# Optimization experiments

Measured on AMD Instinct MI355X. Metric: run time of the kernel, lower is better.

Reference implementation:

```python
import jax, jax.numpy as jnp
import numpy as np

N_NODES = 100000
N_EDGES = 800000
HID = 128
LN_EPS = 1e-5


def _mlp2(x, w1, b1, w2, b2):
    # Linear -> ReLU -> Linear
    return jax.nn.relu(x @ w1 + b1) @ w2 + b2


def setup_inputs() -> dict:
    key = jax.random.key(0)
    ks = jax.random.split(key, 12)
    s = 1.0 / np.sqrt(3 * HID)
    s2 = 1.0 / np.sqrt(HID)
    return {
        "h": jax.random.normal(ks[0], (N_NODES, HID), dtype=jnp.float32),
        "edge_index": jax.random.randint(ks[1], (2, N_EDGES), 0, N_NODES, dtype=jnp.int64),
        "edge_x": jax.random.normal(ks[2], (N_EDGES, HID), dtype=jnp.float32),
        # edge_proj MLP (weights stored [in, out])
        "ep_w1": jax.random.uniform(ks[3], (3 * HID, HID), jnp.float32, -s, s),
        "ep_b1": jax.random.uniform(ks[4], (HID,), jnp.float32, -s, s),
        "ep_w2": jax.random.uniform(ks[5], (HID, HID), jnp.float32, -s2, s2),
        "ep_b2": jax.random.uniform(ks[6], (HID,), jnp.float32, -s2, s2),
        # update MLP
        "up_w1": jax.random.uniform(ks[7], (3 * HID, HID), jnp.float32, -s, s),
        "up_b1": jax.random.uniform(ks[8], (HID,), jnp.float32, -s, s),
        "up_w2": jax.random.uniform(ks[9], (HID, HID), jnp.float32, -s2, s2),
        "up_b2": jax.random.uniform(ks[10], (HID,), jnp.float32, -s2, s2),
        # LayerNorm affine
        "ln_g": jnp.ones((HID,), jnp.float32),
        "ln_b": jnp.zeros((HID,), jnp.float32),
    }


def reference(h, edge_index, edge_x, ep_w1, ep_b1, ep_w2, ep_b2,
              up_w1, up_b1, up_w2, up_b2, ln_g, ln_b):
    n = h.shape[0]
    src, dst = edge_index[0], edge_index[1]
    # edge gather + concat -> [E, 3H] -> message MLP -> [E, H]
    messages = _mlp2(jnp.concatenate([h[src], h[dst], edge_x], axis=-1),
                     ep_w1, ep_b1, ep_w2, ep_b2)
    # scatter-add aggregation for both directions
    incoming = jax.ops.segment_sum(messages, dst, num_segments=n)
    outgoing = jax.ops.segment_sum(messages, src, num_segments=n)
    # degree normalization (clamp min 1)
    ones = jnp.ones((edge_index.shape[1],), h.dtype)
    in_deg = jnp.maximum(jax.ops.segment_sum(ones, dst, num_segments=n), 1.0)[:, None]
    out_deg = jnp.maximum(jax.ops.segment_sum(ones, src, num_segments=n), 1.0)[:, None]
    updated = _mlp2(jnp.concatenate([h, incoming / in_deg, outgoing / out_deg], axis=-1),
                    up_w1, up_b1, up_w2, up_b2)
    # residual + LayerNorm
    x = h + updated
    mu = jnp.mean(x, axis=-1, keepdims=True)
    var = jnp.mean(jnp.square(x - mu), axis=-1, keepdims=True)
    return (x - mu) * jax.lax.rsqrt(var + LN_EPS) * ln_g + ln_b
```

## Files before the change

kernel.cpp:

```cpp
#include <hip/hip_runtime.h>
#include <stdint.h>

#define HIDD 128
#define NNODES 100000
#define NEDGES 800000
#define NSEG 196

typedef short s16x8 __attribute__((ext_vector_type(8)));
typedef float f32x4 __attribute__((ext_vector_type(4)));

__device__ __forceinline__ short f2bf(float f) {
  union { float f; unsigned u; } v; v.f = f;
  return (short)((v.u + 0x7fffu + ((v.u >> 16) & 1u)) >> 16);
}
__device__ __forceinline__ short4 cvt4(float4 v) {
  short4 s; s.x = f2bf(v.x); s.y = f2bf(v.y); s.z = f2bf(v.z); s.w = f2bf(v.w);
  return s;
}
__device__ __forceinline__ float bflo(unsigned w) {
  union { unsigned u; float f; } v; v.u = w << 16; return v.f;
}
__device__ __forceinline__ float bfhi(unsigned w) {
  union { unsigned u; float f; } v; v.u = w & 0xffff0000u; return v.f;
}
__device__ __forceinline__ unsigned pack2(float a, float b) {
  return ((unsigned)(unsigned short)f2bf(b) << 16) | (unsigned)(unsigned short)f2bf(a);
}
__device__ __forceinline__ f32x4 mfma16(s16x8 a, s16x8 b, f32x4 c) {
  return __builtin_amdgcn_mfma_f32_16x16x32_bf16(a, b, c, 0, 0, 0);
}
__device__ __forceinline__ void atomic_pk_bf16(unsigned short* addr, unsigned pk) {
  asm volatile("global_atomic_pk_add_bf16 %0, %1, off" :: "v"(addr), "v"(pk) : "memory");
}

__global__ void k_prep_h(const float4* __restrict__ h4, short4* __restrict__ hb4, int n4) {
  int stride = gridDim.x * blockDim.x;
  for (int i = blockIdx.x * blockDim.x + threadIdx.x; i < n4; i += stride)
    hb4[i] = cvt4(h4[i]);
}

__global__ void k_prep_w(const float* __restrict__ w1e, const float* __restrict__ w2e,
                         const float* __restrict__ w1u, const float* __restrict__ w2u,
                         short* __restrict__ w1et, short* __restrict__ w2et,
                         short* __restrict__ w1ut, short* __restrict__ w2ut) {
  int i = blockIdx.x * 256 + threadIdx.x;
  if (i < 49152) {
    int n = i / 384, k = i - n * 384;
    w1et[i] = f2bf(w1e[k * 128 + n]);
    w1ut[i] = f2bf(w1u[k * 128 + n]);
  } else {
    int j = i - 49152;
    if (j < 16384) {
      int n = j >> 7, k = j & 127;
      int oc = (n & ~31) + 2 * (n & 15) + ((n >> 4) & 1);
      w2et[j] = f2bf(w2e[k * 128 + oc]);
      w2ut[j] = f2bf(w2u[k * 128 + n]);
    }
  }
}

__global__ void k_hist(const int* __restrict__ eidx, int* __restrict__ cnt_s,
                       int* __restrict__ cnt_d) {
  int i = blockIdx.x * 256 + threadIdx.x;
  if (i < NEDGES) {
    atomicAdd(&cnt_s[eidx[i]], 1);
    atomicAdd(&cnt_d[eidx[NEDGES + i]], 1);
  }
}

__global__ void k_bsum(const int* __restrict__ cnt_d, const int* __restrict__ cnt_s,
                       int* __restrict__ bsum) {
  __shared__ int red[256];
  int gb = blockIdx.x, sel = gb >= NSEG, b = gb - sel * NSEG;
  const int* cnt = sel ? cnt_s : cnt_d;
  int t = threadIdx.x;
  int i0 = b * 512 + 2 * t;
  int a = (i0 < NNODES) ? cnt[i0] : 0;
  int c = (i0 + 1 < NNODES) ? cnt[i0 + 1] : 0;
  red[t] = a + c;
  __syncthreads();
  for (int d = 128; d > 0; d >>= 1) {
    if (t < d) red[t] += red[t + d];
    __syncthreads();
  }
  if (t == 0) bsum[gb] = red[0];
}

__global__ void k_soff(int* __restrict__ bsum, int* __restrict__ off_d,
                       int* __restrict__ off_s) {
  if (threadIdx.x == 0) {
    int tot = 0;
    for (int i = 0; i < NSEG; ++i) { int v = bsum[i]; bsum[i] = tot; tot += v; }
    off_d[NNODES] = tot;
  } else if (threadIdx.x == 1) {
    int tot = 0;
    for (int i = NSEG; i < 2 * NSEG; ++i) { int v = bsum[i]; bsum[i] = tot; tot += v; }
    off_s[NNODES] = tot;
  }
}

__global__ void k_sfin(const int* __restrict__ cnt_d, const int* __restrict__ cnt_s,
                       const int* __restrict__ bsum,
                       int* __restrict__ off_d, int* __restrict__ off_s,
                       int* __restrict__ cur_d, int* __restrict__ cur_s) {
  __shared__ int p[256];
  int gb = blockIdx.x, sel = gb >= NSEG, b = gb - sel * NSEG;
  const int* cnt = sel ? cnt_s : cnt_d;
  int* off = sel ? off_s : off_d;
  int* cur = sel ? cur_s : cur_d;
  int t = threadIdx.x;
  int i0 = b * 512 + 2 * t;
  int a = (i0 < NNODES) ? cnt[i0] : 0;
  int c = (i0 + 1 < NNODES) ? cnt[i0 + 1] : 0;
  p[t] = a + c;
  __syncthreads();
  for (int d = 1; d < 256; d <<= 1) {
    int v = (t >= d) ? p[t - d] : 0;
    __syncthreads();
    p[t] += v;
    __syncthreads();
  }
  int excl = (t ? p[t - 1] : 0) + bsum[gb];
  if (i0 < NNODES)     { off[i0] = excl;     cur[i0] = excl; }
  if (i0 + 1 < NNODES) { off[i0 + 1] = excl + a; cur[i0 + 1] = excl + a; }
}

__global__ void k_scat(const int* __restrict__ eidx, int* __restrict__ cur_s,
                       int* __restrict__ cur_d, int* __restrict__ slist,
                       int* __restrict__ dlist) {
  int i = blockIdx.x * 256 + threadIdx.x;
  if (i < NEDGES) {
    slist[atomicAdd(&cur_s[eidx[i]], 1)] = i;
    dlist[atomicAdd(&cur_d[eidx[NEDGES + i]], 1)] = i;
  }
}

__global__ __launch_bounds__(256, 2)
void k_edge2(const short* __restrict__ hb, const int* __restrict__ eidx,
             const float* __restrict__ ex,
             const short* __restrict__ w1t, const short* __restrict__ w2t,
             const float* __restrict__ b1g, const float* __restrict__ b2g,
             unsigned* __restrict__ msgd) {
  __shared__ __align__(16) short Xs[64][392];
  __shared__ __align__(16) short Hs[64][136];

  const int tid = threadIdx.x;
  const int wave = tid >> 6, lane = tid & 63;
  const int lg = lane >> 4, lr = lane & 15;
  const int koff = lg * 8;
  const int c0 = wave * 32 + lr, c1 = c0 + 16;
  const int pc0 = wave * 32 + 2 * lr;

  s16x8 wb1a[12], wb1b[12], wb2a[4], wb2b[4];
#pragma unroll
  for (int kk = 0; kk < 12; ++kk) {
    wb1a[kk] = *(const s16x8*)(w1t + c0 * 384 + kk * 32 + koff);
    wb1b[kk] = *(const s16x8*)(w1t + c1 * 384 + kk * 32 + koff);
  }
#pragma unroll
  for (int kk = 0; kk < 4; ++kk) {
    wb2a[kk] = *(const s16x8*)(w2t + c0 * 128 + kk * 32 + koff);
    wb2b[kk] = *(const s16x8*)(w2t + c1 * 128 + kk * 32 + koff);
  }
  const float bias1_0 = b1g[c0], bias1_1 = b1g[c1];
  const float bias2_0 = b2g[pc0], bias2_1 = b2g[pc0 + 1];

  for (int t = blockIdx.x; t < NEDGES / 64; t += gridDim.x) {
    const int base = t * 64;

    for (int u = tid; u < 64 * 32; u += 256) {
      int r = u >> 5, c = u & 31;
      int node = (c < 16) ? eidx[base + r] : eidx[NEDGES + base + r];
      *(int4*)&Xs[r][c * 8] = *(const int4*)(hb + (long)node * 128 + (c & 15) * 8);
    }
    for (int u = tid; u < 64 * 32; u += 256) {
      int r = u >> 5, q = u & 31;
      float4 v = *(const float4*)(ex + (long)(base + r) * 128 + q * 4);
      *(short4*)&Xs[r][256 + q * 4] = cvt4(v);
    }
    __syncthreads();

    f32x4 acc[4][2] = {};
#pragma unroll
    for (int kk = 0; kk < 12; ++kk) {
      int k0 = kk * 32 + koff;
#pragma unroll
      for (int m = 0; m < 4; ++m) {
        s16x8 a = *(const s16x8*)&Xs[m * 16 + lr][k0];
        acc[m][0] = mfma16(a, wb1a[kk], acc[m][0]);
        acc[m][1] = mfma16(a, wb1b[kk], acc[m][1]);
      }
    }
#pragma unroll
    for (int m = 0; m < 4; ++m)
#pragma unroll
      for (int r2 = 0; r2 < 4; ++r2) {
        int row = m * 16 + lg * 4 + r2;
        Hs[row][c0] = f2bf(fmaxf(acc[m][0][r2] + bias1_0, 0.f));
        Hs[row][c1] = f2bf(fmaxf(acc[m][1][r2] + bias1_1, 0.f));
      }
    __syncthreads();

    f32x4 acc2[4][2] = {};
#pragma unroll
    for (int kk = 0; kk < 4; ++kk) {
#pragma unroll
      for (int m = 0; m < 4; ++m) {
        s16x8 a = *(const s16x8*)&Hs[m * 16 + lr][kk * 32 + koff];
        acc2[m][0] = mfma16(a, wb2a[kk], acc2[m][0]);
        acc2[m][1] = mfma16(a, wb2b[kk], acc2[m][1]);
      }
    }
#pragma unroll
    for (int m = 0; m < 4; ++m)
#pragma unroll
      for (int r2 = 0; r2 < 4; ++r2) {
        int row = m * 16 + lg * 4 + r2;
        msgd[(long)(base + row) * 64 + wave * 16 + lr] =
            pack2(acc2[m][0][r2] + bias2_0, acc2[m][1][r2] + bias2_1);
      }
  }
}

__global__ __launch_bounds__(256, 2)
void k_node2(const float* __restrict__ h, const short* __restrict__ hb,
             const unsigned short* __restrict__ msg,
             const int* __restrict__ off_d, const int* __restrict__ dlist,
             const int* __restrict__ off_s, const int* __restrict__ slist,
             const short* __restrict__ w1t, const short* __restrict__ w2t,
             const float* __restrict__ b1g, const float* __restrict__ b2g,
             const float* __restrict__ lng, const float* __restrict__ lnb,
             float* __restrict__ out) {
  __shared__ __align__(16) char smem[67584];
  short (*Xs)[392] = (short (*)[392])smem;
  float (*Xf)[132] = (float (*)[132])smem;
  short (*Hs)[136] = (short (*)[136])(smem + 50176);

  const int tid = threadIdx.x;
  const int wave = tid >> 6, lane = tid & 63;
  const int lg = lane >> 4, lr = lane & 15;
  const int koff = lg * 8;
  const int c0 = wave * 32 + lr, c1 = c0 + 16;

  s16x8 wb1a[12], wb1b[12], wb2a[4], wb2b[4];
#pragma unroll
  for (int kk = 0; kk < 12; ++kk) {
    wb1a[kk] = *(const s16x8*)(w1t + c0 * 384 + kk * 32 + koff);
    wb1b[kk] = *(const s16x8*)(w1t + c1 * 384 + kk * 32 + koff);
  }
#pragma unroll
  for (int kk = 0; kk < 4; ++kk) {
    wb2a[kk] = *(const s16x8*)(w2t + c0 * 128 + kk * 32 + koff);
    wb2b[kk] = *(const s16x8*)(w2t + c1 * 128 + kk * 32 + koff);
  }
  const float bias1_0 = b1g[c0], bias1_1 = b1g[c1];
  const float bias2_0 = b2g[c0], bias2_1 = b2g[c1];

  const int ntiles = (NNODES + 63) / 64;
  for (int t = blockIdx.x; t < ntiles; t += gridDim.x) {
    const int base = t * 64;

    for (int u = tid; u < 64 * 16; u += 256) {
      int r = u >> 4, c = u & 15;
      long node = min(base + r, NNODES - 1);
      *(int4*)&Xs[r][c * 8] = *(const int4*)(hb + node * 128 + c * 8);
    }
    {
      int r = tid >> 2, q = tid & 3;
      long node = base + r;
      bool valid = node < NNODES;
#pragma unroll
      for (int dir = 0; dir < 2; ++dir) {
        const int* off = dir ? off_s : off_d;
        const int* lst = dir ? slist : dlist;
        float av[32];
#pragma unroll
        for (int j = 0; j < 32; ++j) av[j] = 0.f;
        int e0 = 0, e1 = 0;
        if (valid) { e0 = off[node]; e1 = off[node + 1]; }
        for (int e = e0; e < e1; ++e) {
          int eid = lst[e];
          const uint4* mp = (const uint4*)(msg + (long)eid * 128 + q * 32);
          uint4 u0 = mp[0], u1 = mp[1], u2 = mp[2], u3 = mp[3];
          av[0]  += bflo(u0.x); av[1]  += bfhi(u0.x);
          av[2]  += bflo(u0.y); av[3]  += bfhi(u0.y);
          av[4]  += bflo(u0.z); av[5]  += bfhi(u0.z);
          av[6]  += bflo(u0.w); av[7]  += bfhi(u0.w);
          av[8]  += bflo(u1.x); av[9]  += bfhi(u1.x);
          av[10] += bflo(u1.y); av[11] += bfhi(u1.y);
          av[12] += bflo(u1.z); av[13] += bfhi(u1.z);
          av[14] += bflo(u1.w); av[15] += bfhi(u1.w);
          av[16] += bflo(u2.x); av[17] += bfhi(u2.x);
          av[18] += bflo(u2.y); av[19] += bfhi(u2.y);
          av[20] += bflo(u2.z); av[21] += bfhi(u2.z);
          av[22] += bflo(u2.w); av[23] += bfhi(u2.w);
          av[24] += bflo(u3.x); av[25] += bfhi(u3.x);
          av[26] += bflo(u3.y); av[27] += bfhi(u3.y);
          av[28] += bflo(u3.z); av[29] += bfhi(u3.z);
          av[30] += bflo(u3.w); av[31] += bfhi(u3.w);
        }
        float sc = 1.f / fmaxf((float)(e1 - e0), 1.f);
        unsigned pk[16];
#pragma unroll
        for (int j = 0; j < 16; ++j) pk[j] = pack2(av[2 * j] * sc, av[2 * j + 1] * sc);
        uint4* dst = (uint4*)&Xs[r][(dir ? 256 : 128) + q * 32];
        dst[0] = make_uint4(pk[0], pk[1], pk[2], pk[3]);
        dst[1] = make_uint4(pk[4], pk[5], pk[6], pk[7]);
        dst[2] = make_uint4(pk[8], pk[9], pk[10], pk[11]);
        dst[3] = make_uint4(pk[12], pk[13], pk[14], pk[15]);
      }
    }
    __syncthreads();

    f32x4 acc[4][2] = {};
#pragma unroll
    for (int kk = 0; kk < 12; ++kk) {
      int k0 = kk * 32 + koff;
#pragma unroll
      for (int m = 0; m < 4; ++m) {
        s16x8 a = *(const s16x8*)&Xs[m * 16 + lr][k0];
        acc[m][0] = mfma16(a, wb1a[kk], acc[m][0]);
        acc[m][1] = mfma16(a, wb1b[kk], acc[m][1]);
      }
    }
#pragma unroll
    for (int m = 0; m < 4; ++m)
#pragma unroll
      for (int r2 = 0; r2 < 4; ++r2) {
        int row = m * 16 + lg * 4 + r2;
        Hs[row][c0] = f2bf(fmaxf(acc[m][0][r2] + bias1_0, 0.f));
        Hs[row][c1] = f2bf(fmaxf(acc[m][1][r2] + bias1_1, 0.f));
      }
    __syncthreads();

    f32x4 acc2[4][2] = {};
#pragma unroll
    for (int kk = 0; kk < 4; ++kk) {
      int k0 = kk * 32 + koff;
#pragma unroll
      for (int m = 0; m < 4; ++m) {
        s16x8 a = *(const s16x8*)&Hs[m * 16 + lr][k0];
        acc2[m][0] = mfma16(a, wb2a[kk], acc2[m][0]);
        acc2[m][1] = mfma16(a, wb2b[kk], acc2[m][1]);
      }
    }
#pragma unroll
    for (int m = 0; m < 4; ++m)
#pragma unroll
      for (int r2 = 0; r2 < 4; ++r2) {
        int row = m * 16 + lg * 4 + r2;
        long node = base + row;
        float h0 = 0.f, h1 = 0.f;
        if (node < NNODES) { h0 = h[node * 128 + c0]; h1 = h[node * 128 + c1]; }
        Xf[row][c0] = acc2[m][0][r2] + bias2_0 + h0;
        Xf[row][c1] = acc2[m][1][r2] + bias2_1 + h1;
      }
    __syncthreads();

    {
      int r = tid >> 2, q = tid & 3;
      float sum = 0.f, ss = 0.f;
      float4 vals[8];
#pragma unroll
      for (int j = 0; j < 8; ++j) {
        float4 v = *(const float4*)&Xf[r][q * 32 + j * 4];
        vals[j] = v;
        sum += v.x + v.y + v.z + v.w;
        ss += v.x * v.x + v.y * v.y + v.z * v.z + v.w * v.w;
      }
      sum += __shfl_xor(sum, 1); sum += __shfl_xor(sum, 2);
      ss  += __shfl_xor(ss, 1);  ss  += __shfl_xor(ss, 2);
      float mean = sum * (1.f / 128.f);
      float var = ss * (1.f / 128.f) - mean * mean;
      float rstd = rsqrtf(var + 1e-5f);
      long node = base + r;
      if (node < NNODES) {
#pragma unroll
        for (int j = 0; j < 8; ++j) {
          int cc = q * 32 + j * 4;
          float4 v = vals[j];
          float4 o;
          o.x = (v.x - mean) * rstd * lng[cc + 0] + lnb[cc + 0];
          o.y = (v.y - mean) * rstd * lng[cc + 1] + lnb[cc + 1];
          o.z = (v.z - mean) * rstd * lng[cc + 2] + lnb[cc + 2];
          o.w = (v.w - mean) * rstd * lng[cc + 3] + lnb[cc + 3];
          *(float4*)(out + node * 128 + cc) = o;
        }
      }
    }
    __syncthreads();
  }
}

__global__ __launch_bounds__(256, 2)
void k_edge_at(const short* __restrict__ hb, const int* __restrict__ eidx,
               const float* __restrict__ ex,
               const short* __restrict__ w1t, const short* __restrict__ w2t,
               const float* __restrict__ b1g, const float* __restrict__ b2g,
               unsigned short* __restrict__ incb, unsigned short* __restrict__ outgb,
               float* __restrict__ indeg, float* __restrict__ outdeg) {
  __shared__ __align__(16) short Xs[64][392];
  __shared__ __align__(16) short Hs[64][136];
  const int tid = threadIdx.x;
  const int wave = tid >> 6, lane = tid & 63;
  const int lg = lane >> 4, lr = lane & 15;
  const int koff = lg * 8;
  const int c0 = wave * 32 + lr, c1 = c0 + 16;
  const int pc0 = wave * 32 + 2 * lr;
  s16x8 wb1a[12], wb1b[12], wb2a[4], wb2b[4];
#pragma unroll
  for (int kk = 0; kk < 12; ++kk) {
    wb1a[kk] = *(const s16x8*)(w1t + c0 * 384 + kk * 32 + koff);
    wb1b[kk] = *(const s16x8*)(w1t + c1 * 384 + kk * 32 + koff);
  }
#pragma unroll
  for (int kk = 0; kk < 4; ++kk) {
    wb2a[kk] = *(const s16x8*)(w2t + c0 * 128 + kk * 32 + koff);
    wb2b[kk] = *(const s16x8*)(w2t + c1 * 128 + kk * 32 + koff);
  }
  const float bias1_0 = b1g[c0], bias1_1 = b1g[c1];
  const float bias2_0 = b2g[pc0], bias2_1 = b2g[pc0 + 1];
  for (int t = blockIdx.x; t < NEDGES / 64; t += gridDim.x) {
    const int base = t * 64;
    for (int u = tid; u < 64 * 32; u += 256) {
      int r = u >> 5, c = u & 31;
      int node = (c < 16) ? eidx[base + r] : eidx[NEDGES + base + r];
      *(int4*)&Xs[r][c * 8] = *(const int4*)(hb + (long)node * 128 + (c & 15) * 8);
    }
    for (int u = tid; u < 64 * 32; u += 256) {
      int r = u >> 5, q = u & 31;
      float4 v = *(const float4*)(ex + (long)(base + r) * 128 + q * 4);
      *(short4*)&Xs[r][256 + q * 4] = cvt4(v);
    }
    if (tid < 64) {
      atomicAdd(&outdeg[eidx[base + tid]], 1.0f);
      atomicAdd(&indeg[eidx[NEDGES + base + tid]], 1.0f);
    }
    __syncthreads();
    f32x4 acc[4][2] = {};
#pragma unroll
    for (int kk = 0; kk < 12; ++kk) {
      int k0 = kk * 32 + koff;
#pragma unroll
      for (int m = 0; m < 4; ++m) {
        s16x8 a = *(const s16x8*)&Xs[m * 16 + lr][k0];
        acc[m][0] = mfma16(a, wb1a[kk], acc[m][0]);
        acc[m][1] = mfma16(a, wb1b[kk], acc[m][1]);
      }
    }
#pragma unroll
    for (int m = 0; m < 4; ++m)
#pragma unroll
      for (int r2 = 0; r2 < 4; ++r2) {
        int row = m * 16 + lg * 4 + r2;
        Hs[row][c0] = f2bf(fmaxf(acc[m][0][r2] + bias1_0, 0.f));
        Hs[row][c1] = f2bf(fmaxf(acc[m][1][r2] + bias1_1, 0.f));
      }
    __syncthreads();
    f32x4 acc2[4][2] = {};
#pragma unroll
    for (int kk = 0; kk < 4; ++kk) {
#pragma unroll
      for (int m = 0; m < 4; ++m) {
        s16x8 a = *(const s16x8*)&Hs[m * 16 + lr][kk * 32 + koff];
        acc2[m][0] = mfma16(a, wb2a[kk], acc2[m][0]);
        acc2[m][1] = mfma16(a, wb2b[kk], acc2[m][1]);
      }
    }
#pragma unroll
    for (int m = 0; m < 4; ++m)
#pragma unroll
      for (int r2 = 0; r2 < 4; ++r2) {
        int row = m * 16 + lg * 4 + r2;
        int s = eidx[base + row], d = eidx[NEDGES + base + row];
        unsigned pk = pack2(acc2[m][0][r2] + bias2_0, acc2[m][1][r2] + bias2_1);
        atomic_pk_bf16(outgb + (long)s * 128 + pc0, pk);
        atomic_pk_bf16(incb + (long)d * 128 + pc0, pk);
      }
  }
}

__global__ __launch_bounds__(256, 2)
void k_node_at(const float* __restrict__ h, const short* __restrict__ hb,
               const unsigned short* __restrict__ incb,
               const unsigned short* __restrict__ outgb,
               const float* __restrict__ indeg, const float* __restrict__ outdeg,
               const short* __restrict__ w1t, const short* __restrict__ w2t,
               const float* __restrict__ b1g, const float* __restrict__ b2g,
               const float* __restrict__ lng, const float* __restrict__ lnb,
               float* __restrict__ out) {
  __shared__ __align__(16) char smem[67584];
  short (*Xs)[392] = (short (*)[392])smem;
  float (*Xf)[132] = (float (*)[132])smem;
  short (*Hs)[136] = (short (*)[136])(smem + 50176);
  const int tid = threadIdx.x;
  const int wave = tid >> 6, lane = tid & 63;
  const int lg = lane >> 4, lr = lane & 15;
  const int koff = lg * 8;
  const int c0 = wave * 32 + lr, c1 = c0 + 16;
  s16x8 wb1a[12], wb1b[12], wb2a[4], wb2b[4];
#pragma unroll
  for (int kk = 0; kk < 12; ++kk) {
    wb1a[kk] = *(const s16x8*)(w1t + c0 * 384 + kk * 32 + koff);
    wb1b[kk] = *(const s16x8*)(w1t + c1 * 384 + kk * 32 + koff);
  }
#pragma unroll
  for (int kk = 0; kk < 4; ++kk) {
    wb2a[kk] = *(const s16x8*)(w2t + c0 * 128 + kk * 32 + koff);
    wb2b[kk] = *(const s16x8*)(w2t + c1 * 128 + kk * 32 + koff);
  }
  const float bias1_0 = b1g[c0], bias1_1 = b1g[c1];
  const float bias2_0 = b2g[c0], bias2_1 = b2g[c1];
  const int ntiles = (NNODES + 63) / 64;
  for (int t = blockIdx.x; t < ntiles; t += gridDim.x) {
    const int base = t * 64;
    for (int u = tid; u < 64 * 16; u += 256) {
      int r = u >> 4, c = u & 15;
      long node = min(base + r, NNODES - 1);
      *(int4*)&Xs[r][c * 8] = *(const int4*)(hb + node * 128 + c * 8);
    }
    for (int u = tid; u < 64 * 16; u += 256) {
      int r = u >> 4, c = u & 15;
      long node = min(base + r, NNODES - 1);
      float s = 1.f / fmaxf(indeg[node], 1.f);
      uint4 w = *(const uint4*)(incb + node * 128 + c * 8);
      *(uint4*)&Xs[r][128 + c * 8] = make_uint4(
        pack2(bflo(w.x) * s, bfhi(w.x) * s), pack2(bflo(w.y) * s, bfhi(w.y) * s),
        pack2(bflo(w.z) * s, bfhi(w.z) * s), pack2(bflo(w.w) * s, bfhi(w.w) * s));
    }
    for (int u = tid; u < 64 * 16; u += 256) {
      int r = u >> 4, c = u & 15;
      long node = min(base + r, NNODES - 1);
      float s = 1.f / fmaxf(outdeg[node], 1.f);
      uint4 w = *(const uint4*)(outgb + node * 128 + c * 8);
      *(uint4*)&Xs[r][256 + c * 8] = make_uint4(
        pack2(bflo(w.x) * s, bfhi(w.x) * s), pack2(bflo(w.y) * s, bfhi(w.y) * s),
        pack2(bflo(w.z) * s, bfhi(w.z) * s), pack2(bflo(w.w) * s, bfhi(w.w) * s));
    }
    __syncthreads();
    f32x4 acc[4][2] = {};
#pragma unroll
    for (int kk = 0; kk < 12; ++kk) {
      int k0 = kk * 32 + koff;
#pragma unroll
      for (int m = 0; m < 4; ++m) {
        s16x8 a = *(const s16x8*)&Xs[m * 16 + lr][k0];
        acc[m][0] = mfma16(a, wb1a[kk], acc[m][0]);
        acc[m][1] = mfma16(a, wb1b[kk], acc[m][1]);
      }
    }
#pragma unroll
    for (int m = 0; m < 4; ++m)
#pragma unroll
      for (int r2 = 0; r2 < 4; ++r2) {
        int row = m * 16 + lg * 4 + r2;
        Hs[row][c0] = f2bf(fmaxf(acc[m][0][r2] + bias1_0, 0.f));
        Hs[row][c1] = f2bf(fmaxf(acc[m][1][r2] + bias1_1, 0.f));
      }
    __syncthreads();
    f32x4 acc2[4][2] = {};
#pragma unroll
    for (int kk = 0; kk < 4; ++kk) {
      int k0 = kk * 32 + koff;
#pragma unroll
      for (int m = 0; m < 4; ++m) {
        s16x8 a = *(const s16x8*)&Hs[m * 16 + lr][k0];
        acc2[m][0] = mfma16(a, wb2a[kk], acc2[m][0]);
        acc2[m][1] = mfma16(a, wb2b[kk], acc2[m][1]);
      }
    }
#pragma unroll
    for (int m = 0; m < 4; ++m)
#pragma unroll
      for (int r2 = 0; r2 < 4; ++r2) {
        int row = m * 16 + lg * 4 + r2;
        long node = base + row;
        float h0 = 0.f, h1 = 0.f;
        if (node < NNODES) { h0 = h[node * 128 + c0]; h1 = h[node * 128 + c1]; }
        Xf[row][c0] = acc2[m][0][r2] + bias2_0 + h0;
        Xf[row][c1] = acc2[m][1][r2] + bias2_1 + h1;
      }
    __syncthreads();
    {
      int r = tid >> 2, q = tid & 3;
      float sum = 0.f, ss = 0.f;
      float4 vals[8];
#pragma unroll
      for (int j = 0; j < 8; ++j) {
        float4 v = *(const float4*)&Xf[r][q * 32 + j * 4];
        vals[j] = v;
        sum += v.x + v.y + v.z + v.w;
        ss += v.x * v.x + v.y * v.y + v.z * v.z + v.w * v.w;
      }
      sum += __shfl_xor(sum, 1); sum += __shfl_xor(sum, 2);
      ss  += __shfl_xor(ss, 1);  ss  += __shfl_xor(ss, 2);
      float mean = sum * (1.f / 128.f);
      float var = ss * (1.f / 128.f) - mean * mean;
      float rstd = rsqrtf(var + 1e-5f);
      long node = base + r;
      if (node < NNODES) {
#pragma unroll
        for (int j = 0; j < 8; ++j) {
          int cc = q * 32 + j * 4;
          float4 v = vals[j];
          float4 o;
          o.x = (v.x - mean) * rstd * lng[cc + 0] + lnb[cc + 0];
          o.y = (v.y - mean) * rstd * lng[cc + 1] + lnb[cc + 1];
          o.z = (v.z - mean) * rstd * lng[cc + 2] + lnb[cc + 2];
          o.w = (v.w - mean) * rstd * lng[cc + 3] + lnb[cc + 3];
          *(float4*)(out + node * 128 + cc) = o;
        }
      }
    }
    __syncthreads();
  }
}

extern "C" void kernel_launch(void* const* d_in, const int* in_sizes, int n_in,
                              void* d_out, int out_size, void* d_ws, size_t ws_size,
                              hipStream_t stream) {
  const float* h    = (const float*)d_in[0];
  const int*   ei   = (const int*)d_in[1];
  const float* ex   = (const float*)d_in[2];
  const float* epw1 = (const float*)d_in[3];
  const float* epb1 = (const float*)d_in[4];
  const float* epw2 = (const float*)d_in[5];
  const float* epb2 = (const float*)d_in[6];
  const float* upw1 = (const float*)d_in[7];
  const float* upb1 = (const float*)d_in[8];
  const float* upw2 = (const float*)d_in[9];
  const float* upb2 = (const float*)d_in[10];
  const float* lng  = (const float*)d_in[11];
  const float* lnb  = (const float*)d_in[12];
  float* out = (float*)d_out;
  char* ws = (char*)d_ws;

  const size_t NEED = 239500000;
  if (ws_size >= NEED) {
    unsigned short* msg = (unsigned short*)(ws);
    short* hb    = (short*)(ws + 204800000);
    short* w1et  = (short*)(ws + 230400000);
    short* w2et  = (short*)(ws + 230498304);
    short* w1ut  = (short*)(ws + 230531072);
    short* w2ut  = (short*)(ws + 230629376);
    int* cnt_d   = (int*)(ws + 230662144);
    int* cnt_s   = (int*)(ws + 231062144);
    int* off_d   = (int*)(ws + 231462144);
    int* off_s   = (int*)(ws + 231862148);
    int* cur_d   = (int*)(ws + 232262152);
    int* cur_s   = (int*)(ws + 232662152);
    int* dlist   = (int*)(ws + 233062152);
    int* slist   = (int*)(ws + 236262152);
    int* bsum    = (int*)(ws + 239462152);

    hipMemsetAsync(cnt_d, 0, 800000, stream);
    hipLaunchKernelGGL(k_prep_h, dim3(2048), dim3(256), 0, stream,
                       (const float4*)h, (short4*)hb, NNODES * 128 / 4);
    hipLaunchKernelGGL(k_prep_w, dim3(256), dim3(256), 0, stream,
                       epw1, epw2, upw1, upw2, w1et, w2et, w1ut, w2ut);
    hipLaunchKernelGGL(k_hist, dim3((NEDGES + 255) / 256), dim3(256), 0, stream,
                       ei, cnt_s, cnt_d);
    hipLaunchKernelGGL(k_bsum, dim3(2 * NSEG), dim3(256), 0, stream,
                       cnt_d, cnt_s, bsum);
    hipLaunchKernelGGL(k_soff, dim3(1), dim3(64), 0, stream, bsum, off_d, off_s);
    hipLaunchKernelGGL(k_sfin, dim3(2 * NSEG), dim3(256), 0, stream,
                       cnt_d, cnt_s, bsum, off_d, off_s, cur_d, cur_s);
    hipLaunchKernelGGL(k_scat, dim3((NEDGES + 255) / 256), dim3(256), 0, stream,
                       ei, cur_s, cur_d, slist, dlist);
    hipLaunchKernelGGL(k_edge2, dim3(1024), dim3(256), 0, stream,
                       hb, ei, ex, w1et, w2et, epb1, epb2, (unsigned*)msg);
    hipLaunchKernelGGL(k_node2, dim3(512), dim3(256), 0, stream,
                       h, hb, msg, off_d, dlist, off_s, slist,
                       w1ut, w2ut, upb1, upb2, lng, lnb, out);
  } else {
    unsigned short* incb  = (unsigned short*)(ws);
    unsigned short* outgb = (unsigned short*)(ws + 25600000);
    float* indeg  = (float*)(ws + 51200000);
    float* outdeg = (float*)(ws + 51600000);
    short* hb     = (short*)(ws + 52000000);
    short* w1et   = (short*)(ws + 77600000);
    short* w2et   = (short*)(ws + 77698304);
    short* w1ut   = (short*)(ws + 77731072);
    short* w2ut   = (short*)(ws + 77829376);

    hipMemsetAsync(ws, 0, 52000000, stream);
    hipLaunchKernelGGL(k_prep_h, dim3(2048), dim3(256), 0, stream,
                       (const float4*)h, (short4*)hb, NNODES * 128 / 4);
    hipLaunchKernelGGL(k_prep_w, dim3(256), dim3(256), 0, stream,
                       epw1, epw2, upw1, upw2, w1et, w2et, w1ut, w2ut);
    hipLaunchKernelGGL(k_edge_at, dim3(1024), dim3(256), 0, stream,
                       hb, ei, ex, w1et, w2et, epb1, epb2, incb, outgb, indeg, outdeg);
    hipLaunchKernelGGL(k_node_at, dim3(512), dim3(256), 0, stream,
                       h, hb, incb, outgb, indeg, outdeg, w1ut, w2ut, upb1, upb2,
                       lng, lnb, out);
  }
}
```

Before: 756.3 us.

## Scatter messages into CSR-ordered buffers per direction to avoid indirect gathers

The scatter pass now records each edge's slot in the src- and dst-sorted orders instead of building edge lists. The edge MLP kernel writes each message twice, directly into per-direction buffers in CSR order. The node kernel then streams contiguous message rows per node without looking up edge ids. This removes the dependent index load and random gathers, but doubles the message writes as scattered rows and roughly doubles the workspace requirement.

```diff
diff --git a/kernel.cpp b/kernel.cpp
--- a/kernel.cpp
+++ b/kernel.cpp
@@ -125,13 +125,13 @@
   if (i0 + 1 < NNODES) { off[i0 + 1] = excl + a; cur[i0 + 1] = excl + a; }
 }
 
-__global__ void k_scat(const int* __restrict__ eidx, int* __restrict__ cur_s,
-                       int* __restrict__ cur_d, int* __restrict__ slist,
-                       int* __restrict__ dlist) {
+__global__ void k_scat2(const int* __restrict__ eidx, int* __restrict__ cur_s,
+                        int* __restrict__ cur_d, int* __restrict__ slot_s,
+                        int* __restrict__ slot_d) {
   int i = blockIdx.x * 256 + threadIdx.x;
   if (i < NEDGES) {
-    slist[atomicAdd(&cur_s[eidx[i]], 1)] = i;
-    dlist[atomicAdd(&cur_d[eidx[NEDGES + i]], 1)] = i;
+    slot_s[i] = atomicAdd(&cur_s[eidx[i]], 1);
+    slot_d[i] = atomicAdd(&cur_d[eidx[NEDGES + i]], 1);
   }
 }
 
@@ -140,9 +140,11 @@
              const float* __restrict__ ex,
              const short* __restrict__ w1t, const short* __restrict__ w2t,
              const float* __restrict__ b1g, const float* __restrict__ b2g,
-             unsigned* __restrict__ msgd) {
+             const int* __restrict__ slot_s, const int* __restrict__ slot_d,
+             unsigned* __restrict__ msg_s, unsigned* __restrict__ msg_d) {
   __shared__ __align__(16) short Xs[64][392];
   __shared__ __align__(16) short Hs[64][136];
+  __shared__ int Ss[64], Sd[64];
 
   const int tid = threadIdx.x;
   const int wave = tid >> 6, lane = tid & 63;
@@ -178,6 +180,8 @@
       float4 v = *(const float4*)(ex + (long)(base + r) * 128 + q * 4);
       *(short4*)&Xs[r][256 + q * 4] = cvt4(v);
     }
+    if (tid < 64) Ss[tid] = slot_s[base + tid];
+    else if (tid < 128) Sd[tid - 64] = slot_d[base + tid - 64];
     __syncthreads();
 
     f32x4 acc[4][2] = {};
@@ -216,17 +220,19 @@
 #pragma unroll
       for (int r2 = 0; r2 < 4; ++r2) {
         int row = m * 16 + lg * 4 + r2;
-        msgd[(long)(base + row) * 64 + wave * 16 + lr] =
-            pack2(acc2[m][0][r2] + bias2_0, acc2[m][1][r2] + bias2_1);
-      }
+        unsigned pk = pack2(acc2[m][0][r2] + bias2_0, acc2[m][1][r2] + bias2_1);
+        int lo = wave * 16 + lr;
+        msg_s[(long)Ss[row] * 64 + lo] = pk;
+        msg_d[(long)Sd[row] * 64 + lo] = pk;
+      }
+    __syncthreads();
   }
 }
 
 __global__ __launch_bounds__(256, 2)
 void k_node2(const float* __restrict__ h, const short* __restrict__ hb,
-             const unsigned short* __restrict__ msg,
-             const int* __restrict__ off_d, const int* __restrict__ dlist,
-             const int* __restrict__ off_s, const int* __restrict__ slist,
+             const unsigned* __restrict__ msg_d, const int* __restrict__ off_d,
+             const unsigned* __restrict__ msg_s, const int* __restrict__ off_s,
              const short* __restrict__ w1t, const short* __restrict__ w2t,
              const float* __restrict__ b1g, const float* __restrict__ b2g,
              const float* __restrict__ lng, const float* __restrict__ lnb,
@@ -272,15 +278,14 @@
 #pragma unroll
       for (int dir = 0; dir < 2; ++dir) {
         const int* off = dir ? off_s : off_d;
-        const int* lst = dir ? slist : dlist;
+        const unsigned* msg = dir ? msg_s : msg_d;
         float av[32];
 #pragma unroll
         for (int j = 0; j < 32; ++j) av[j] = 0.f;
         int e0 = 0, e1 = 0;
         if (valid) { e0 = off[node]; e1 = off[node + 1]; }
         for (int e = e0; e < e1; ++e) {
-          int eid = lst[e];
-          const uint4* mp = (const uint4*)(msg + (long)eid * 128 + q * 32);
+          const uint4* mp = (const uint4*)(msg + (long)e * 64 + q * 16);
           uint4 u0 = mp[0], u1 = mp[1], u2 = mp[2], u3 = mp[3];
           av[0]  += bflo(u0.x); av[1]  += bfhi(u0.x);
           av[2]  += bflo(u0.y); av[3]  += bfhi(u0.y);
@@ -635,23 +640,24 @@
   float* out = (float*)d_out;
   char* ws = (char*)d_ws;
 
-  const size_t NEED = 239500000;
+  const size_t NEED = 444300000ULL;
   if (ws_size >= NEED) {
-    unsigned short* msg = (unsigned short*)(ws);
-    short* hb    = (short*)(ws + 204800000);
-    short* w1et  = (short*)(ws + 230400000);
-    short* w2et  = (short*)(ws + 230498304);
-    short* w1ut  = (short*)(ws + 230531072);
-    short* w2ut  = (short*)(ws + 230629376);
-    int* cnt_d   = (int*)(ws + 230662144);
-    int* cnt_s   = (int*)(ws + 231062144);
-    int* off_d   = (int*)(ws + 231462144);
-    int* off_s   = (int*)(ws + 231862148);
-    int* cur_d   = (int*)(ws + 232262152);
-    int* cur_s   = (int*)(ws + 232662152);
-    int* dlist   = (int*)(ws + 233062152);
-    int* slist   = (int*)(ws + 236262152);
-    int* bsum    = (int*)(ws + 239462152);
+    unsigned* msg_s = (unsigned*)(ws);
+    unsigned* msg_d = (unsigned*)(ws + 204800000);
+    short* hb    = (short*)(ws + 409600000);
+    short* w1et  = (short*)(ws + 435200000);
+    short* w2et  = (short*)(ws + 435298304);
+    short* w1ut  = (short*)(ws + 435331072);
+    short* w2ut  = (short*)(ws + 435429376);
+    int* cnt_d   = (int*)(ws + 435462144);
+    int* cnt_s   = (int*)(ws + 435862144);
+    int* off_d   = (int*)(ws + 436262144);
+    int* off_s   = (int*)(ws + 436662148);
+    int* cur_d   = (int*)(ws + 437062152);
+    int* cur_s   = (int*)(ws + 437462152);
+    int* slot_s  = (int*)(ws + 437862152);
+    int* slot_d  = (int*)(ws + 441062152);
+    int* bsum    = (int*)(ws + 444262152);
 
     hipMemsetAsync(cnt_d, 0, 800000, stream);
     hipLaunchKernelGGL(k_prep_h, dim3(2048), dim3(256), 0, stream,
@@ -665,12 +671,13 @@
     hipLaunchKernelGGL(k_soff, dim3(1), dim3(64), 0, stream, bsum, off_d, off_s);
     hipLaunchKernelGGL(k_sfin, dim3(2 * NSEG), dim3(256), 0, stream,
                        cnt_d, cnt_s, bsum, off_d, off_s, cur_d, cur_s);
-    hipLaunchKernelGGL(k_scat, dim3((NEDGES + 255) / 256), dim3(256), 0, stream,
-                       ei, cur_s, cur_d, slist, dlist);
+    hipLaunchKernelGGL(k_scat2, dim3((NEDGES + 255) / 256), dim3(256), 0, stream,
+                       ei, cur_s, cur_d, slot_s, slot_d);
     hipLaunchKernelGGL(k_edge2, dim3(1024), dim3(256), 0, stream,
-                       hb, ei, ex, w1et, w2et, epb1, epb2, (unsigned*)msg);
+                       hb, ei, ex, w1et, w2et, epb1, epb2, slot_s, slot_d,
+                       msg_s, msg_d);
     hipLaunchKernelGGL(k_node2, dim3(512), dim3(256), 0, stream,
-                       h, hb, msg, off_d, dlist, off_s, slist,
+                       h, hb, msg_d, off_d, msg_s, off_s,
                        w1ut, w2ut, upb1, upb2, lng, lnb, out);
   } else {
     unsigned short* incb  = (unsigned short*)(ws);
```

Result: faster. 721.4 us (-4.6%).

## Process edges in dst-sorted order; scatter outgoing messages via packed bf16 atomics

Applied to the files above, without the earlier changes.

The edge kernel now walks edges in destination-sorted order, so messages are stored contiguously per destination. The node kernel can then read incoming messages sequentially without an index indirection. Outgoing aggregation no longer needs a src CSR: the edge kernel atomically adds packed bf16 pairs into a per-node buffer, and the node kernel scales that buffer by the src degree. This drops the src scan and scatter kernels and the random message gathers, but adds bf16 atomic contention, reduced-precision accumulation, a 25.6 MB memset and gathered edge_x reads.

```diff
diff --git a/kernel.cpp b/kernel.cpp
--- a/kernel.cpp
+++ b/kernel.cpp
@@ -68,50 +68,36 @@
   }
 }
 
-__global__ void k_bsum(const int* __restrict__ cnt_d, const int* __restrict__ cnt_s,
-                       int* __restrict__ bsum) {
+__global__ void k_bsum_d(const int* __restrict__ cnt_d, int* __restrict__ bsum) {
   __shared__ int red[256];
-  int gb = blockIdx.x, sel = gb >= NSEG, b = gb - sel * NSEG;
-  const int* cnt = sel ? cnt_s : cnt_d;
-  int t = threadIdx.x;
+  int b = blockIdx.x, t = threadIdx.x;
   int i0 = b * 512 + 2 * t;
-  int a = (i0 < NNODES) ? cnt[i0] : 0;
-  int c = (i0 + 1 < NNODES) ? cnt[i0 + 1] : 0;
+  int a = (i0 < NNODES) ? cnt_d[i0] : 0;
+  int c = (i0 + 1 < NNODES) ? cnt_d[i0 + 1] : 0;
   red[t] = a + c;
   __syncthreads();
   for (int d = 128; d > 0; d >>= 1) {
     if (t < d) red[t] += red[t + d];
     __syncthreads();
   }
-  if (t == 0) bsum[gb] = red[0];
-}
-
-__global__ void k_soff(int* __restrict__ bsum, int* __restrict__ off_d,
-                       int* __restrict__ off_s) {
+  if (t == 0) bsum[b] = red[0];
+}
+
+__global__ void k_soff_d(int* __restrict__ bsum, int* __restrict__ off_d) {
   if (threadIdx.x == 0) {
     int tot = 0;
     for (int i = 0; i < NSEG; ++i) { int v = bsum[i]; bsum[i] = tot; tot += v; }
     off_d[NNODES] = tot;
-  } else if (threadIdx.x == 1) {
-    int tot = 0;
-    for (int i = NSEG; i < 2 * NSEG; ++i) { int v = bsum[i]; bsum[i] = tot; tot += v; }
-    off_s[NNODES] = tot;
-  }
-}
-
-__global__ void k_sfin(const int* __restrict__ cnt_d, const int* __restrict__ cnt_s,
-                       const int* __restrict__ bsum,
-                       int* __restrict__ off_d, int* __restrict__ off_s,
-                       int* __restrict__ cur_d, int* __restrict__ cur_s) {
+  }
+}
+
+__global__ void k_sfin_d(const int* __restrict__ cnt_d, const int* __restrict__ bsum,
+                         int* __restrict__ off_d, int* __restrict__ cur_d) {
   __shared__ int p[256];
-  int gb = blockIdx.x, sel = gb >= NSEG, b = gb - sel * NSEG;
-  const int* cnt = sel ? cnt_s : cnt_d;
-  int* off = sel ? off_s : off_d;
-  int* cur = sel ? cur_s : cur_d;
-  int t = threadIdx.x;
+  int b = blockIdx.x, t = threadIdx.x;
   int i0 = b * 512 + 2 * t;
-  int a = (i0 < NNODES) ? cnt[i0] : 0;
-  int c = (i0 + 1 < NNODES) ? cnt[i0 + 1] : 0;
+  int a = (i0 < NNODES) ? cnt_d[i0] : 0;
+  int c = (i0 + 1 < NNODES) ? cnt_d[i0 + 1] : 0;
   p[t] = a + c;
   __syncthreads();
   for (int d = 1; d < 256; d <<= 1) {
@@ -120,29 +106,27 @@
     p[t] += v;
     __syncthreads();
   }
-  int excl = (t ? p[t - 1] : 0) + bsum[gb];
-  if (i0 < NNODES)     { off[i0] = excl;     cur[i0] = excl; }
-  if (i0 + 1 < NNODES) { off[i0 + 1] = excl + a; cur[i0 + 1] = excl + a; }
-}
-
-__global__ void k_scat(const int* __restrict__ eidx, int* __restrict__ cur_s,
-                       int* __restrict__ cur_d, int* __restrict__ slist,
-                       int* __restrict__ dlist) {
+  int excl = (t ? p[t - 1] : 0) + bsum[b];
+  if (i0 < NNODES)     { off_d[i0] = excl;     cur_d[i0] = excl; }
+  if (i0 + 1 < NNODES) { off_d[i0 + 1] = excl + a; cur_d[i0 + 1] = excl + a; }
+}
+
+__global__ void k_scat_d(const int* __restrict__ eidx, int* __restrict__ cur_d,
+                         int* __restrict__ dlist) {
   int i = blockIdx.x * 256 + threadIdx.x;
-  if (i < NEDGES) {
-    slist[atomicAdd(&cur_s[eidx[i]], 1)] = i;
-    dlist[atomicAdd(&cur_d[eidx[NEDGES + i]], 1)] = i;
-  }
+  if (i < NEDGES) dlist[atomicAdd(&cur_d[eidx[NEDGES + i]], 1)] = i;
 }
 
 __global__ __launch_bounds__(256, 2)
-void k_edge2(const short* __restrict__ hb, const int* __restrict__ eidx,
+void k_edge3(const short* __restrict__ hb, const int* __restrict__ eidx,
              const float* __restrict__ ex,
              const short* __restrict__ w1t, const short* __restrict__ w2t,
              const float* __restrict__ b1g, const float* __restrict__ b2g,
-             unsigned* __restrict__ msgd) {
+             const int* __restrict__ dlist,
+             unsigned* __restrict__ msg_d, unsigned short* __restrict__ outgb) {
   __shared__ __align__(16) short Xs[64][392];
   __shared__ __align__(16) short Hs[64][136];
+  __shared__ int Es[64], Ss[64];
 
   const int tid = threadIdx.x;
   const int wave = tid >> 6, lane = tid & 63;
@@ -168,16 +152,22 @@
   for (int t = blockIdx.x; t < NEDGES / 64; t += gridDim.x) {
     const int base = t * 64;
 
+    int myeid = 0;
+    if (tid < 64) { myeid = dlist[base + tid]; Es[tid] = myeid; }
+    __syncthreads();
+
     for (int u = tid; u < 64 * 32; u += 256) {
       int r = u >> 5, c = u & 31;
-      int node = (c < 16) ? eidx[base + r] : eidx[NEDGES + base + r];
+      int eid = Es[r];
+      int node = (c < 16) ? eidx[eid] : eidx[NEDGES + eid];
       *(int4*)&Xs[r][c * 8] = *(const int4*)(hb + (long)node * 128 + (c & 15) * 8);
     }
     for (int u = tid; u < 64 * 32; u += 256) {
       int r = u >> 5, q = u & 31;
-      float4 v = *(const float4*)(ex + (long)(base + r) * 128 + q * 4);
+      float4 v = *(const float4*)(ex + (long)Es[r] * 128 + q * 4);
       *(short4*)&Xs[r][256 + q * 4] = cvt4(v);
     }
+    if (tid < 64) Ss[tid] = eidx[myeid];
     __syncthreads();
 
     f32x4 acc[4][2] = {};
@@ -204,9 +194,10 @@
     f32x4 acc2[4][2] = {};
 #pragma unroll
     for (int kk = 0; kk < 4; ++kk) {
-#pragma unroll
-      for (int m = 0; m < 4; ++m) {
-        s16x8 a = *(const s16x8*)&Hs[m * 16 + lr][kk * 32 + koff];
+      int k0 = kk * 32 + koff;
+#pragma unroll
+      for (int m = 0; m < 4; ++m) {
+        s16x8 a = *(const s16x8*)&Hs[m * 16 + lr][k0];
         acc2[m][0] = mfma16(a, wb2a[kk], acc2[m][0]);
         acc2[m][1] = mfma16(a, wb2b[kk], acc2[m][1]);
       }
@@ -216,17 +207,17 @@
 #pragma unroll
       for (int r2 = 0; r2 < 4; ++r2) {
         int row = m * 16 + lg * 4 + r2;
-        msgd[(long)(base + row) * 64 + wave * 16 + lr] =
-            pack2(acc2[m][0][r2] + bias2_0, acc2[m][1][r2] + bias2_1);
+        unsigned pk = pack2(acc2[m][0][r2] + bias2_0, acc2[m][1][r2] + bias2_1);
+        msg_d[(long)(base + row) * 64 + wave * 16 + lr] = pk;
+        atomic_pk_bf16(outgb + (long)Ss[row] * 128 + pc0, pk);
       }
   }
 }
 
 __global__ __launch_bounds__(256, 2)
-void k_node2(const float* __restrict__ h, const short* __restrict__ hb,
-             const unsigned short* __restrict__ msg,
-             const int* __restrict__ off_d, const int* __restrict__ dlist,
-             const int* __restrict__ off_s, const int* __restrict__ slist,
+void k_node3(const float* __restrict__ h, const short* __restrict__ hb,
+             const unsigned* __restrict__ msg_d, const int* __restrict__ off_d,
+             const unsigned short* __restrict__ outgb, const int* __restrict__ cnt_s,
              const short* __restrict__ w1t, const short* __restrict__ w2t,
              const float* __restrict__ b1g, const float* __restrict__ b2g,
              const float* __restrict__ lng, const float* __restrict__ lnb,
@@ -256,6 +247,16 @@
   const float bias1_0 = b1g[c0], bias1_1 = b1g[c1];
   const float bias2_0 = b2g[c0], bias2_1 = b2g[c1];
 
+#define ACCUM(u0,u1,u2,u3) \
+  av[0]+=bflo(u0.x); av[1]+=bfhi(u0.x); av[2]+=bflo(u0.y); av[3]+=bfhi(u0.y); \
+  av[4]+=bflo(u0.z); av[5]+=bfhi(u0.z); av[6]+=bflo(u0.w); av[7]+=bfhi(u0.w); \
+  av[8]+=bflo(u1.x); av[9]+=bfhi(u1.x); av[10]+=bflo(u1.y); av[11]+=bfhi(u1.y); \
+  av[12]+=bflo(u1.z); av[13]+=bfhi(u1.z); av[14]+=bflo(u1.w); av[15]+=bfhi(u1.w); \
+  av[16]+=bflo(u2.x); av[17]+=bfhi(u2.x); av[18]+=bflo(u2.y); av[19]+=bfhi(u2.y); \
+  av[20]+=bflo(u2.z); av[21]+=bfhi(u2.z); av[22]+=bflo(u2.w); av[23]+=bfhi(u2.w); \
+  av[24]+=bflo(u3.x); av[25]+=bfhi(u3.x); av[26]+=bflo(u3.y); av[27]+=bfhi(u3.y); \
+  av[28]+=bflo(u3.z); av[29]+=bfhi(u3.z); av[30]+=bflo(u3.w); av[31]+=bfhi(u3.w);
+
   const int ntiles = (NNODES + 63) / 64;
   for (int t = blockIdx.x; t < ntiles; t += gridDim.x) {
     const int base = t * 64;
@@ -265,50 +266,47 @@
       long node = min(base + r, NNODES - 1);
       *(int4*)&Xs[r][c * 8] = *(const int4*)(hb + node * 128 + c * 8);
     }
+    for (int u = tid; u < 64 * 16; u += 256) {
+      int r = u >> 4, c = u & 15;
+      long node = min(base + r, NNODES - 1);
+      float s = 1.f / fmaxf((float)cnt_s[node], 1.f);
+      uint4 w = *(const uint4*)(outgb + node * 128 + c * 8);
+      *(uint4*)&Xs[r][256 + c * 8] = make_uint4(
+        pack2(bflo(w.x) * s, bfhi(w.x) * s), pack2(bflo(w.y) * s, bfhi(w.y) * s),
+        pack2(bflo(w.z) * s, bfhi(w.z) * s), pack2(bflo(w.w) * s, bfhi(w.w) * s));
+    }
     {
       int r = tid >> 2, q = tid & 3;
       long node = base + r;
       bool valid = node < NNODES;
-#pragma unroll
-      for (int dir = 0; dir < 2; ++dir) {
-        const int* off = dir ? off_s : off_d;
-        const int* lst = dir ? slist : dlist;
-        float av[32];
-#pragma unroll
-        for (int j = 0; j < 32; ++j) av[j] = 0.f;
-        int e0 = 0, e1 = 0;
-        if (valid) { e0 = off[node]; e1 = off[node + 1]; }
-        for (int e = e0; e < e1; ++e) {
-          int eid = lst[e];
-          const uint4* mp = (const uint4*)(msg + (long)eid * 128 + q * 32);
-          uint4 u0 = mp[0], u1 = mp[1], u2 = mp[2], u3 = mp[3];
-          av[0]  += bflo(u0.x); av[1]  += bfhi(u0.x);
-          av[2]  += bflo(u0.y); av[3]  += bfhi(u0.y);
-          av[4]  += bflo(u0.z); av[5]  += bfhi(u0.z);
-          av[6]  += bflo(u0.w); av[7]  += bfhi(u0.w);
-          av[8]  += bflo(u1.x); av[9]  += bfhi(u1.x);
-          av[10] += bflo(u1.y); av[11] += bfhi(u1.y);
-          av[12] += bflo(u1.z); av[13] += bfhi(u1.z);
-          av[14] += bflo(u1.w); av[15] += bfhi(u1.w);
-          av[16] += bflo(u2.x); av[17] += bfhi(u2.x);
-          av[18] += bflo(u2.y); av[19] += bfhi(u2.y);
-          av[20] += bflo(u2.z); av[21] += bfhi(u2.z);
-          av[22] += bflo(u2.w); av[23] += bfhi(u2.w);
-          av[24] += bflo(u3.x); av[25] += bfhi(u3.x);
-          av[26] += bflo(u3.y); av[27] += bfhi(u3.y);
-          av[28] += bflo(u3.z); av[29] += bfhi(u3.z);
-          av[30] += bflo(u3.w); av[31] += bfhi(u3.w);
-        }
-        float sc = 1.f / fmaxf((float)(e1 - e0), 1.f);
-        unsigned pk[16];
-#pragma unroll
-        for (int j = 0; j < 16; ++j) pk[j] = pack2(av[2 * j] * sc, av[2 * j + 1] * sc);
-        uint4* dst = (uint4*)&Xs[r][(dir ? 256 : 128) + q * 32];
-        dst[0] = make_uint4(pk[0], pk[1], pk[2], pk[3]);
-        dst[1] = make_uint4(pk[4], pk[5], pk[6], pk[7]);
-        dst[2] = make_uint4(pk[8], pk[9], pk[10], pk[11]);
-        dst[3] = make_uint4(pk[12], pk[13], pk[14], pk[15]);
-      }
+      float av[32];
+#pragma unroll
+      for (int j = 0; j < 32; ++j) av[j] = 0.f;
+      int e0 = 0, e1 = 0;
+      if (valid) { e0 = off_d[node]; e1 = off_d[node + 1]; }
+      int e = e0;
+      for (; e + 1 < e1; e += 2) {
+        const uint4* mp0 = (const uint4*)(msg_d + (long)e * 64 + q * 16);
+        const uint4* mp1 = (const uint4*)(msg_d + (long)(e + 1) * 64 + q * 16);
+        uint4 a0 = mp0[0], a1 = mp0[1], a2 = mp0[2], a3 = mp0[3];
+        uint4 b0 = mp1[0], b1 = mp1[1], b2 = mp1[2], b3 = mp1[3];
+        ACCUM(a0, a1, a2, a3)
+        ACCUM(b0, b1, b2, b3)
+      }
+      if (e < e1) {
+        const uint4* mp0 = (const uint4*)(msg_d + (long)e * 64 + q * 16);
+        uint4 a0 = mp0[0], a1 = mp0[1], a2 = mp0[2], a3 = mp0[3];
+        ACCUM(a0, a1, a2, a3)
+      }
+      float sc = 1.f / fmaxf((float)(e1 - e0), 1.f);
+      unsigned pk[16];
+#pragma unroll
+      for (int j = 0; j < 16; ++j) pk[j] = pack2(av[2 * j] * sc, av[2 * j + 1] * sc);
+      uint4* dst = (uint4*)&Xs[r][128 + q * 32];
+      dst[0] = make_uint4(pk[0], pk[1], pk[2], pk[3]);
+      dst[1] = make_uint4(pk[4], pk[5], pk[6], pk[7]);
+      dst[2] = make_uint4(pk[8], pk[9], pk[10], pk[11]);
+      dst[3] = make_uint4(pk[12], pk[13], pk[14], pk[15]);
     }
     __syncthreads();
 
@@ -390,6 +388,7 @@
     }
     __syncthreads();
   }
+#undef ACCUM
 }
 
 __global__ __launch_bounds__(256, 2)
@@ -635,24 +634,23 @@
   float* out = (float*)d_out;
   char* ws = (char*)d_ws;
 
-  const size_t NEED = 239500000;
+  const size_t NEED = 261100000ULL;
   if (ws_size >= NEED) {
-    unsigned short* msg = (unsigned short*)(ws);
-    short* hb    = (short*)(ws + 204800000);
-    short* w1et  = (short*)(ws + 230400000);
-    short* w2et  = (short*)(ws + 230498304);
-    short* w1ut  = (short*)(ws + 230531072);
-    short* w2ut  = (short*)(ws + 230629376);
-    int* cnt_d   = (int*)(ws + 230662144);
-    int* cnt_s   = (int*)(ws + 231062144);
-    int* off_d   = (int*)(ws + 231462144);
-    int* off_s   = (int*)(ws + 231862148);
-    int* cur_d   = (int*)(ws + 232262152);
-    int* cur_s   = (int*)(ws + 232662152);
-    int* dlist   = (int*)(ws + 233062152);
-    int* slist   = (int*)(ws + 236262152);
-    int* bsum    = (int*)(ws + 239462152);
-
+    unsigned* msg_d = (unsigned*)(ws);
+    unsigned short* outgb = (unsigned short*)(ws + 204800000);
+    short* hb    = (short*)(ws + 230400000);
+    short* w1et  = (short*)(ws + 256000000);
+    short* w2et  = (short*)(ws + 256098304);
+    short* w1ut  = (short*)(ws + 256131072);
+    short* w2ut  = (short*)(ws + 256229376);
+    int* cnt_d   = (int*)(ws + 256262144);
+    int* cnt_s   = (int*)(ws + 256662144);
+    int* off_d   = (int*)(ws + 257062144);
+    int* cur_d   = (int*)(ws + 257462148);
+    int* dlist   = (int*)(ws + 257862148);
+    int* bsum    = (int*)(ws + 261062148);
+
+    hipMemsetAsync(outgb, 0, 25600000, stream);
     hipMemsetAsync(cnt_d, 0, 800000, stream);
     hipLaunchKernelGGL(k_prep_h, dim3(2048), dim3(256), 0, stream,
                        (const float4*)h, (short4*)hb, NNODES * 128 / 4);
@@ -660,17 +658,16 @@
                        epw1, epw2, upw1, upw2, w1et, w2et, w1ut, w2ut);
     hipLaunchKernelGGL(k_hist, dim3((NEDGES + 255) / 256), dim3(256), 0, stream,
                        ei, cnt_s, cnt_d);
-    hipLaunchKernelGGL(k_bsum, dim3(2 * NSEG), dim3(256), 0, stream,
-                       cnt_d, cnt_s, bsum);
-    hipLaunchKernelGGL(k_soff, dim3(1), dim3(64), 0, stream, bsum, off_d, off_s);
-    hipLaunchKernelGGL(k_sfin, dim3(2 * NSEG), dim3(256), 0, stream,
-                       cnt_d, cnt_s, bsum, off_d, off_s, cur_d, cur_s);
-    hipLaunchKernelGGL(k_scat, dim3((NEDGES + 255) / 256), dim3(256), 0, stream,
-                       ei, cur_s, cur_d, slist, dlist);
-    hipLaunchKernelGGL(k_edge2, dim3(1024), dim3(256), 0, stream,
-                       hb, ei, ex, w1et, w2et, epb1, epb2, (unsigned*)msg);
-    hipLaunchKernelGGL(k_node2, dim3(512), dim3(256), 0, stream,
-                       h, hb, msg, off_d, dlist, off_s, slist,
+    hipLaunchKernelGGL(k_bsum_d, dim3(NSEG), dim3(256), 0, stream, cnt_d, bsum);
+    hipLaunchKernelGGL(k_soff_d, dim3(1), dim3(64), 0, stream, bsum, off_d);
+    hipLaunchKernelGGL(k_sfin_d, dim3(NSEG), dim3(256), 0, stream,
+                       cnt_d, bsum, off_d, cur_d);
+    hipLaunchKernelGGL(k_scat_d, dim3((NEDGES + 255) / 256), dim3(256), 0, stream,
+                       ei, cur_d, dlist);
+    hipLaunchKernelGGL(k_edge3, dim3(1024), dim3(256), 0, stream,
+                       hb, ei, ex, w1et, w2et, epb1, epb2, dlist, msg_d, outgb);
+    hipLaunchKernelGGL(k_node3, dim3(512), dim3(256), 0, stream,
+                       h, hb, msg_d, off_d, outgb, cnt_s,
                        w1ut, w2ut, upb1, upb2, lng, lnb, out);
   } else {
     unsigned short* incb  = (unsigned short*)(ws);
```

New measurement: 730.3 us. 1.04x faster.
